# Optimization experiments

Hardware: AMD Instinct MI355X
Metric: run time of the kernel (lower is better)

## Reference

```python
import jax, jax.numpy as jnp
import numpy as np

B, S, D = 4, 2048, 768
H = 12
DH = D // H
NUM_WAY = 4
DFF = 4 * D  # FFN expansion scale=4
EPS = 1e-6


def setup_inputs() -> dict:
    key = jax.random.key(0)
    ks = jax.random.split(key, 20)
    s = 0.02
    inp = {
        "x": jax.random.normal(ks[0], (B, S, D), jnp.float32),
        "w": jax.random.randint(ks[1], (B, S), 0, NUM_WAY, jnp.int64),
        # LayerNorm 1
        "ln1_g": jnp.ones((D,), jnp.float32),
        "ln1_b": jnp.zeros((D,), jnp.float32),
        # Multi-head attention projections (input_dim=out_dim=D)
        "wq": jax.random.normal(ks[2], (D, D), jnp.float32) * s,
        "bq": jnp.zeros((D,), jnp.float32),
        "wk": jax.random.normal(ks[3], (D, D), jnp.float32) * s,
        "bk": jnp.zeros((D,), jnp.float32),
        "wv": jax.random.normal(ks[4], (D, D), jnp.float32) * s,
        "bv": jnp.zeros((D,), jnp.float32),
        "wo": jax.random.normal(ks[5], (D, D), jnp.float32) * s,
        "bo": jnp.zeros((D,), jnp.float32),
        # Way classifier
        "wcls": jax.random.normal(ks[6], (D, NUM_WAY), jnp.float32) * s,
        "bcls": jnp.zeros((NUM_WAY,), jnp.float32),
        # num_way stacked FFN experts: Linear(D,4D) -> ReLU -> Linear(4D,D)
        "w1": jax.random.normal(ks[7], (NUM_WAY, D, DFF), jnp.float32) * s,
        "b1": jnp.zeros((NUM_WAY, DFF), jnp.float32),
        "w2": jax.random.normal(ks[8], (NUM_WAY, DFF, D), jnp.float32) * s,
        "b2": jnp.zeros((NUM_WAY, D), jnp.float32),
    }
    return inp


def _layernorm(x, g, b):
    mu = jnp.mean(x, axis=-1, keepdims=True)
    var = jnp.mean(jnp.square(x - mu), axis=-1, keepdims=True)
    return (x - mu) * jax.lax.rsqrt(var + EPS) * g + b


def reference(x, w, ln1_g, ln1_b, wq, bq, wk, bk, wv, bv, wo, bo,
              wcls, bcls, w1, b1, w2, b2):
    # pre-LN
    xn = _layernorm(x, ln1_g, ln1_b)
    # multi-head self-attention (q = k = v = xn)
    q = (xn @ wq + bq).reshape(B, S, H, DH)
    k = (xn @ wk + bk).reshape(B, S, H, DH)
    v = (xn @ wv + bv).reshape(B, S, H, DH)
    scores = jnp.einsum('bqhd,bkhd->bhqk', q, k) / jnp.sqrt(jnp.float32(DH))
    attn = jax.nn.softmax(scores, axis=-1)
    ctx = jnp.einsum('bhqk,bkhd->bqhd', attn, v).reshape(B, S, D)
    ctx = ctx @ wo + bo
    # dropout is identity at inference; residual
    out = ctx + x
    # dense compute-all-experts FFN, then per-token select by routing id w
    # (mask-overwrite in original == one-hot select since masks partition)
    ffn_out = jnp.zeros_like(out)
    for ci in range(NUM_WAY):
        h = jax.nn.relu(out @ w1[ci] + b1[ci])        # [B,S,4D]
        fi = h @ w2[ci] + b2[ci]                      # [B,S,D]
        mask = (w == ci).astype(out.dtype)[..., None]  # [B,S,1]
        if ci == 0:
            # original initializes ffn_out with way-0 output everywhere;
            # later ways overwrite where w == ci, net = select expert w
            ffn_out = fi
        else:
            ffn_out = ffn_out * (1.0 - mask) + fi * mask
    way_logits = out @ wcls + bcls  # [B,S,NUM_WAY]
    return ffn_out, way_logits
```

## Files before the change

kernel.cpp:

```cpp
#include <hip/hip_runtime.h>
#include <cstdint>

typedef unsigned short u16;
typedef float f32x4 __attribute__((ext_vector_type(4)));
typedef float f32x16 __attribute__((ext_vector_type(16)));
typedef __bf16 bf16x8 __attribute__((ext_vector_type(8)));

#define LOG2E 1.44269504088896340736f

__device__ __forceinline__ u16 f2bf(float f) {
    union { float f; unsigned u; } v; v.f = f;
    unsigned r = v.u + 0x7fffu + ((v.u >> 16) & 1u);
    return (u16)(r >> 16);
}

__device__ __forceinline__ unsigned cvt_pk_bf16(float lo, float hi) {
    unsigned r;
    asm("v_cvt_pk_bf16_f32 %0, %1, %2" : "=v"(r) : "v"(lo), "v"(hi));
    return r;
}

__device__ __forceinline__ float exp2_hw(float x) {
    float r;
    asm("v_exp_f32 %0, %1" : "=v"(r) : "v"(x));
    return r;
}

__device__ __forceinline__ f32x4 mfma16(bf16x8 a, bf16x8 b, f32x4 c) {
    return __builtin_amdgcn_mfma_f32_16x16x32_bf16(a, b, c, 0, 0, 0);
}

__device__ __forceinline__ f32x16 mfma32(bf16x8 a, bf16x8 b, f32x16 c) {
    return __builtin_amdgcn_mfma_f32_32x32x16_bf16(a, b, c, 0, 0, 0);
}

__device__ __forceinline__ void gload_lds16(const void* g, void* l) {
    __builtin_amdgcn_global_load_lds(
        (__attribute__((address_space(1))) unsigned int*)(g),
        (__attribute__((address_space(3))) unsigned int*)(l),
        16, 0, 0);
}

#define MB_TOK 8192
#define DM 768
#define HH 12
#define DHD 64
#define NWAY 4
#define DFF 3072
#define SEQ 2048
#define NBATCH 4

__global__ __launch_bounds__(256) void ln_kernel(
    const float* __restrict__ x, const float* __restrict__ g,
    const float* __restrict__ bb, u16* __restrict__ xn)
{
    int row = blockIdx.x, t = threadIdx.x;
    const float* xr = x + (size_t)row * DM;
    float v0 = xr[t], v1 = xr[t + 256], v2 = xr[t + 512];
    float s = v0 + v1 + v2;
    __shared__ float red[4];
    #pragma unroll
    for (int k = 1; k < 64; k <<= 1) s += __shfl_xor(s, k);
    if ((t & 63) == 0) red[t >> 6] = s;
    __syncthreads();
    float mu = (red[0] + red[1] + red[2] + red[3]) * (1.f / 768.f);
    float d0 = v0 - mu, d1 = v1 - mu, d2 = v2 - mu;
    float q = d0 * d0 + d1 * d1 + d2 * d2;
    #pragma unroll
    for (int k = 1; k < 64; k <<= 1) q += __shfl_xor(q, k);
    __syncthreads();
    if ((t & 63) == 0) red[t >> 6] = q;
    __syncthreads();
    float var = (red[0] + red[1] + red[2] + red[3]) * (1.f / 768.f);
    float rs = rsqrtf(var + 1e-6f);
    u16* xo = xn + (size_t)row * DM;
    xo[t]       = f2bf(d0 * rs * g[t]       + bb[t]);
    xo[t + 256] = f2bf(d1 * rs * g[t + 256] + bb[t + 256]);
    xo[t + 512] = f2bf(d2 * rs * g[t + 512] + bb[t + 512]);
}

__global__ __launch_bounds__(256) void transpose_bf16(
    const float* __restrict__ src, u16* __restrict__ dst, int K, int N)
{
    __shared__ float tl[32][33];
    size_t bofs = (size_t)blockIdx.z * K * N;
    src += bofs; dst += bofs;
    int n0 = blockIdx.x * 32, k0 = blockIdx.y * 32;
    int tx = threadIdx.x, ty = threadIdx.y;
    #pragma unroll
    for (int j = 0; j < 4; ++j)
        tl[ty + j * 8][tx] = src[(size_t)(k0 + ty + j * 8) * N + n0 + tx];
    __syncthreads();
    #pragma unroll
    for (int j = 0; j < 4; ++j)
        dst[(size_t)(n0 + ty + j * 8) * K + k0 + tx] = f2bf(tl[tx][ty + j * 8]);
}

__global__ __launch_bounds__(256) void vT_kernel(
    const u16* __restrict__ qkv, u16* __restrict__ vT)
{
    __shared__ u16 tl[32][33];
    int bh = blockIdx.z;
    int b = bh / HH, h = bh % HH;
    int key0 = blockIdx.x * 32;
    int d0 = blockIdx.y * 32;
    int tx = threadIdx.x, ty = threadIdx.y;
    const u16* src = qkv + ((size_t)b * SEQ + key0) * 2304 + 1536 + h * 64 + d0;
    #pragma unroll
    for (int j = 0; j < 4; ++j)
        tl[ty + j * 8][tx] = src[(size_t)(ty + j * 8) * 2304 + tx];
    __syncthreads();
    u16* dst = vT + ((size_t)bh * 64 + d0) * SEQ + key0;
    #pragma unroll
    for (int j = 0; j < 4; ++j)
        dst[(size_t)(ty + j * 8) * SEQ + tx] = tl[tx][ty + j * 8];
}

__global__ void concat_bias_kernel(const float* bq, const float* bk,
                                   const float* bv, float* bqkv)
{
    int i = blockIdx.x * 256 + threadIdx.x;
    if (i < 2304) bqkv[i] = i < 768 ? bq[i] : (i < 1536 ? bk[i - 768] : bv[i - 1536]);
}

__global__ void route_kernel(const int* __restrict__ wl,
                             int* __restrict__ perm, int* __restrict__ eoff,
                             int4* __restrict__ fmap, int4* __restrict__ fmap64)
{
    __shared__ int cnt[4], cur[4], off[5];
    int tid = threadIdx.x;
    if (tid < 4) cnt[tid] = 0;
    __syncthreads();
    for (int t = tid; t < MB_TOK; t += 256) atomicAdd(&cnt[wl[t] & 3], 1);
    __syncthreads();
    if (tid == 0) {
        off[0] = 0;
        for (int e = 0; e < 4; ++e) off[e + 1] = off[e] + cnt[e];
        int idx = 0;
        for (int e = 0; e < 4; ++e)
            for (int s = 0; s < cnt[e]; s += 128)
                fmap[idx++] = make_int4(e, off[e], s, cnt[e] - s);
        for (; idx < 72; ++idx) fmap[idx] = make_int4(-1, 0, 0, 0);
        int idx2 = 0;
        for (int e = 0; e < 4; ++e)
            for (int s = 0; s < cnt[e]; s += 64)
                fmap64[idx2++] = make_int4(e, off[e], s, cnt[e] - s);
        for (; idx2 < 136; ++idx2) fmap64[idx2] = make_int4(-1, 0, 0, 0);
        for (int e = 0; e < 5; ++e) eoff[e] = off[e];
        for (int e = 0; e < 4; ++e) cur[e] = off[e];
    }
    __syncthreads();
    for (int t = tid; t < MB_TOK; t += 256) {
        int e = wl[t] & 3;
        int pos = atomicAdd(&cur[e], 1);
        perm[pos] = t;
    }
}

template<int MODE, int TM, bool RELU, bool RES, bool ST32, bool ST16>
__global__ __launch_bounds__(256, (TM == 64) ? 4 : 3) void gemm_bt_kernel(
    const u16* __restrict__ A, const u16* __restrict__ Bt,
    const float* __restrict__ bias, const float* __restrict__ res,
    float* __restrict__ out32, u16* __restrict__ out16,
    int nbt, int N, int K, int ntn,
    const int* __restrict__ perm, const int4* __restrict__ fmap)
{
    constexpr int ALD = TM * 32;
    constexpr int BLD = 128 * 32;
    constexpr int NLD = (TM == 128) ? 4 : 3;
    constexpr int NN  = (TM == 64) ? 2 : 4;
    __shared__ __attribute__((aligned(16))) u16 As[3][ALD];
    __shared__ __attribute__((aligned(16))) u16 Bs[3][BLD];
    int tid = threadIdx.x;
    int wv = tid >> 6, ln = tid & 63;
    int bpx = gridDim.x / (ntn << 3);
    int jj = blockIdx.x >> 3;
    int bt = (blockIdx.x & 7) * bpx + jj / ntn;
    int tn = (jj % ntn) * 128;
    if (bt >= nbt) return;

    int seg = 0, ms = 0, mb = TM, tm = 0;
    if (MODE != 0) {
        int4 ent = fmap[bt];
        if (ent.x < 0) return;
        seg = ent.y; ms = ent.z; mb = ent.w; if (mb > TM) mb = TM;
        Bt += (size_t)ent.x * N * K;
        bias += ent.x * N;
    } else {
        tm = bt * TM;
    }

    f32x4 acc[4][NN];
    #pragma unroll
    for (int i = 0; i < 4; ++i)
        #pragma unroll
        for (int j = 0; j < NN; ++j) acc[i][j] = f32x4{0.f, 0.f, 0.f, 0.f};

    int wr = (TM == 128) ? (wv >> 1) : 0;
    int wcol0 = (TM == 128) ? (wv & 1) * 64 : wv * 32;
    int lr = ln & 15, hi = ln >> 4;
    int nk = K / 32;

    const u16* asrc[2];
    const u16* bsrc[2];
    #pragma unroll
    for (int i = 0; i < 2; ++i) {
        int rb2 = (TM == 128) ? ((wv * 2 + i) * 16 + (ln >> 2))
                              : (wv * 16 + (ln >> 2));
        if (TM == 128 || i == 0) {
            int am = rb2 < mb ? rb2 : (mb - 1);
            size_t arow;
            if (MODE == 1)      arow = (size_t)perm[seg + ms + am];
            else if (MODE == 2) arow = (size_t)(seg + ms + am);
            else                arow = (size_t)(tm + rb2);
            asrc[i] = A + arow * K + (ln & 3) * 8;
        }
        int rB = (wv * 2 + i) * 16 + (ln >> 2);
        bsrc[i] = Bt + (size_t)(tn + rB) * K + (ln & 3) * 8;
    }
    int aofs0 = (TM == 128) ? (wv * 2) * 512 : wv * 512;
    int bofs0 = (wv * 2) * 512, bofs1 = (wv * 2 + 1) * 512;

#define GSTAGE(ab_, bb_, k0_) do {                                        \
    gload_lds16(asrc[0] + (k0_), (ab_) + aofs0);                          \
    if (TM == 128) gload_lds16(asrc[1] + (k0_), (ab_) + aofs0 + 512);     \
    gload_lds16(bsrc[0] + (k0_), (bb_) + bofs0);                          \
    gload_lds16(bsrc[1] + (k0_), (bb_) + bofs1);                          \
} while (0)

    u16* A0 = &As[0][0];
    u16* B0 = &Bs[0][0];
    GSTAGE(A0, B0, 0);
    GSTAGE(A0 + ALD, B0 + BLD, 32);
    int bf3 = 0;
    for (int kk = 0; kk < nk; ++kk) {
        if (kk + 1 < nk)
            asm volatile("s_waitcnt vmcnt(%0) lgkmcnt(0)" :: "i"(NLD) : "memory");
        else
            asm volatile("s_waitcnt vmcnt(0) lgkmcnt(0)" ::: "memory");
        __builtin_amdgcn_s_barrier();
        __builtin_amdgcn_sched_barrier(0);
        if (kk + 2 < nk) {
            int nb = bf3 + 2; if (nb >= 3) nb -= 3;
            GSTAGE(A0 + nb * ALD, B0 + nb * BLD, (kk + 2) * 32);
        }
        const u16* Ab = A0 + bf3 * ALD;
        const u16* Bb = B0 + bf3 * BLD;
        bf16x8 a[4], b[NN];
        #pragma unroll
        for (int m = 0; m < 4; ++m)
            a[m] = *(const bf16x8*)&Ab[(wr * 64 + m * 16 + lr) * 32 + hi * 8];
        #pragma unroll
        for (int n = 0; n < NN; ++n)
            b[n] = *(const bf16x8*)&Bb[(wcol0 + n * 16 + lr) * 32 + hi * 8];
        #pragma unroll
        for (int m = 0; m < 4; ++m)
            #pragma unroll
            for (int n = 0; n < NN; ++n)
                acc[m][n] = mfma16(a[m], b[n], acc[m][n]);
        bf3 = (bf3 == 2) ? 0 : bf3 + 1;
    }
#undef GSTAGE

    #pragma unroll
    for (int m = 0; m < 4; ++m) {
        int rb = wr * 64 + m * 16 + hi * 4;
        #pragma unroll
        for (int n = 0; n < NN; ++n) {
            int gcol = tn + wcol0 + n * 16 + lr;
            float bvv = bias[gcol];
            #pragma unroll
            for (int i = 0; i < 4; ++i) {
                int rml = rb + i;
                float v = acc[m][n][i] + bvv;
                if (RELU) v = v > 0.f ? v : 0.f;
                if (MODE == 0) {
                    size_t grow = (size_t)(tm + rml);
                    if (RES) v += res[grow * N + gcol];
                    if (ST32) out32[grow * N + gcol] = v;
                    if (ST16) out16[grow * N + gcol] = f2bf(v);
                } else {
                    if (rml < mb) {
                        size_t orow = (MODE == 1) ? (size_t)(seg + ms + rml)
                                                  : (size_t)perm[seg + ms + rml];
                        if (ST32) out32[orow * N + gcol] = v;
                        if (ST16) out16[orow * N + gcol] = f2bf(v);
                    }
                }
            }
        }
    }
}

__global__ __launch_bounds__(256, 4) void attn_kernel(
    const u16* __restrict__ qkv, const u16* __restrict__ vT,
    u16* __restrict__ ctx)
{
    __shared__ __attribute__((aligned(16))) u16 Ks[2][4096];
    __shared__ __attribute__((aligned(16))) u16 Vs[2][4096];
    int tid = threadIdx.x;
    int wv = tid >> 6, ln = tid & 63;
    int qv = ln & 31, hi = ln >> 5;
    int bid = blockIdx.x;
    int bh = (bid & 7) * 6 + ((bid >> 3) % 6);
    int qt = (bid >> 3) / 6;
    int b = bh / HH, h = bh % HH;
    int q0 = qt * 128 + wv * 32;
    size_t qrowb = (size_t)(b * SEQ + q0);
    const float C = 0.125f * LOG2E;

    bf16x8 qf[4];
    {
        const u16* qp = qkv + (qrowb + qv) * 2304 + h * 64 + hi * 8;
        #pragma unroll
        for (int ds = 0; ds < 4; ++ds) qf[ds] = *(const bf16x8*)(qp + ds * 16);
    }

    int csrc = 8 * ((ln & 7) ^ (ln >> 3));
    const size_t kbase = (size_t)b * SEQ * 2304 + 768 + h * 64;
    const u16* vtb = vT + (size_t)bh * 64 * SEQ;
    const u16* kp0 = qkv + kbase + (size_t)(wv * 16 + (ln >> 3)) * 2304 + csrc;
    const u16* kp1 = kp0 + (size_t)8 * 2304;
    const u16* vp0 = vtb + (size_t)(wv * 16 + (ln >> 3)) * SEQ + csrc;
    const u16* vp1 = vp0 + (size_t)8 * SEQ;

#define ATTN_STAGE(bf_, t_) do {                                          \
    gload_lds16(kp0 + (size_t)(t_) * 64 * 2304, &Ks[bf_][(wv * 2) * 512]);\
    gload_lds16(kp1 + (size_t)(t_) * 64 * 2304, &Ks[bf_][(wv * 2 + 1) * 512]);\
    gload_lds16(vp0 + (size_t)(t_) * 64, &Vs[bf_][(wv * 2) * 512]);       \
    gload_lds16(vp1 + (size_t)(t_) * 64, &Vs[bf_][(wv * 2 + 1) * 512]);   \
} while (0)

    f32x16 oacc[2];
    #pragma unroll
    for (int i = 0; i < 2; ++i)
        #pragma unroll
        for (int r = 0; r < 16; ++r) oacc[i][r] = 0.f;
    float m_run = -INFINITY, l_run = 0.f;
    int ksw = (qv & 7) * 8;

    ATTN_STAGE(0, 0);

    for (int kt = 0; kt < SEQ / 64; ++kt) {
        int bf = kt & 1;
        __syncthreads();
        if (kt + 1 < SEQ / 64) ATTN_STAGE(bf ^ 1, kt + 1);

        f32x16 s0, s1;
        #pragma unroll
        for (int r = 0; r < 16; ++r) { s0[r] = 0.f; s1[r] = 0.f; }
        #pragma unroll
        for (int ds = 0; ds < 4; ++ds) {
            bf16x8 ka0 = *(const bf16x8*)&Ks[bf][qv * 64 + ((ds * 16 + hi * 8) ^ ksw)];
            bf16x8 ka1 = *(const bf16x8*)&Ks[bf][(32 + qv) * 64 + ((ds * 16 + hi * 8) ^ ksw)];
            s0 = mfma32(ka0, qf[ds], s0);
            s1 = mfma32(ka1, qf[ds], s1);
        }

        float tmax = s0[0];
        #pragma unroll
        for (int r = 1; r < 16; ++r) tmax = fmaxf(tmax, s0[r]);
        #pragma unroll
        for (int r = 0; r < 16; ++r) tmax = fmaxf(tmax, s1[r]);
        tmax = fmaxf(tmax, __shfl_xor(tmax, 32));

        if (!__all(tmax - m_run <= 64.f)) {
            float m_new = fmaxf(m_run, tmax);
            float corr = exp2_hw((m_run - m_new) * C);
            l_run *= corr;
            #pragma unroll
            for (int i = 0; i < 2; ++i)
                #pragma unroll
                for (int r = 0; r < 16; ++r) oacc[i][r] *= corr;
            m_run = m_new;
        }
        float c2 = -m_run * C;
        float psum = 0.f;
        #pragma unroll
        for (int r = 0; r < 16; ++r) {
            s0[r] = exp2_hw(fmaf(s0[r], C, c2)); psum += s0[r];
            s1[r] = exp2_hw(fmaf(s1[r], C, c2)); psum += s1[r];
        }
        l_run += psum;

        #pragma unroll
        for (int kb = 0; kb < 2; ++kb) {
            #pragma unroll
            for (int hc = 0; hc < 2; ++hc) {
                const f32x16& sv = kb ? s1 : s0;
                unsigned x0 = cvt_pk_bf16(sv[8 * hc + 0], sv[8 * hc + 1]);
                unsigned x1 = cvt_pk_bf16(sv[8 * hc + 2], sv[8 * hc + 3]);
                unsigned x2 = cvt_pk_bf16(sv[8 * hc + 4], sv[8 * hc + 5]);
                unsigned x3 = cvt_pk_bf16(sv[8 * hc + 6], sv[8 * hc + 7]);
                unsigned t0 = hi ? x0 : x2, t1 = hi ? x1 : x3;
                unsigned r0 = (unsigned)__shfl_xor((int)t0, 32);
                unsigned r1 = (unsigned)__shfl_xor((int)t1, 32);
                union { bf16x8 v; unsigned u[4]; } pf;
                pf.u[0] = hi ? r0 : x0; pf.u[1] = hi ? r1 : x1;
                pf.u[2] = hi ? x2 : r0; pf.u[3] = hi ? x3 : r1;
                int kc = (kb * 32 + hc * 16 + hi * 8) ^ ksw;
                #pragma unroll
                for (int dblk = 0; dblk < 2; ++dblk) {
                    bf16x8 va = *(const bf16x8*)&Vs[bf][(dblk * 32 + qv) * 64 + kc];
                    oacc[dblk] = mfma32(va, pf.v, oacc[dblk]);
                }
            }
        }
    }
#undef ATTN_STAGE

    float l_tot = l_run + __shfl_xor(l_run, 32);
    float inv = 1.f / l_tot;

    __syncthreads();
    u16* eb = &Ks[0][0] + wv * 2048;
    #pragma unroll
    for (int dblk = 0; dblk < 2; ++dblk)
        #pragma unroll
        for (int r = 0; r < 16; r += 2) {
            int d = dblk * 32 + (r & 3) + 8 * (r >> 2) + 4 * hi;
            unsigned pk = cvt_pk_bf16(oacc[dblk][r] * inv, oacc[dblk][r + 1] * inv);
            *(unsigned*)&eb[qv * 64 + (d ^ ((qv & 7) * 8))] = pk;
        }
    __syncthreads();
    {
        u16* ctr = ctx + (qrowb + qv) * DM + h * 64 + hi * 32;
        #pragma unroll
        for (int g = 0; g < 4; ++g) {
            bf16x8 vv = *(const bf16x8*)&eb[qv * 64 + ((hi * 32 + g * 8) ^ ((qv & 7) * 8))];
            *(bf16x8*)(ctr + g * 8) = vv;
        }
    }
}

__global__ __launch_bounds__(256) void cls_kernel(
    const float* __restrict__ outm, const float* __restrict__ wcls,
    const float* __restrict__ bcls, float* __restrict__ dst)
{
    int row = blockIdx.x, t = threadIdx.x;
    const float* xr = outm + (size_t)row * DM;
    float a0 = 0, a1 = 0, a2 = 0, a3 = 0;
    for (int j = t; j < DM; j += 256) {
        float xv = xr[j];
        float4 wv4 = *(const float4*)(const void*)(wcls + (size_t)j * 4);
        a0 += xv * wv4.x; a1 += xv * wv4.y; a2 += xv * wv4.z; a3 += xv * wv4.w;
    }
    #pragma unroll
    for (int k = 1; k < 64; k <<= 1) {
        a0 += __shfl_xor(a0, k); a1 += __shfl_xor(a1, k);
        a2 += __shfl_xor(a2, k); a3 += __shfl_xor(a3, k);
    }
    __shared__ float red[4][4];
    if ((t & 63) == 0) {
        int wid = t >> 6;
        red[wid][0] = a0; red[wid][1] = a1; red[wid][2] = a2; red[wid][3] = a3;
    }
    __syncthreads();
    if (t < 4)
        dst[(size_t)row * 4 + t] =
            red[0][t] + red[1][t] + red[2][t] + red[3][t] + bcls[t];
}

extern "C" void kernel_launch(void* const* d_in, const int* in_sizes, int n_in,
                              void* d_out, int out_size, void* d_ws, size_t ws_size,
                              hipStream_t stream) {
    const float* x      = (const float*)d_in[0];
    const int*   wl     = (const int*)d_in[1];
    const float* ln_g   = (const float*)d_in[2];
    const float* ln_b   = (const float*)d_in[3];
    const float* wq     = (const float*)d_in[4];
    const float* bq     = (const float*)d_in[5];
    const float* wk     = (const float*)d_in[6];
    const float* bk     = (const float*)d_in[7];
    const float* wvv    = (const float*)d_in[8];
    const float* bv     = (const float*)d_in[9];
    const float* wo     = (const float*)d_in[10];
    const float* bo     = (const float*)d_in[11];
    const float* wcls   = (const float*)d_in[12];
    const float* bcls   = (const float*)d_in[13];
    const float* w1     = (const float*)d_in[14];
    const float* b1     = (const float*)d_in[15];
    const float* w2     = (const float*)d_in[16];
    const float* b2     = (const float*)d_in[17];
    float* out = (float*)d_out;

    char* ws = (char*)d_ws;
    u16*   xn    = (u16*)  (ws + 0);
    u16*   qkv   = (u16*)  (ws + 12582912);
    u16*   hbuf  = (u16*)  (ws + 0);
    u16*   ctx   = (u16*)  (ws + 50331648);
    u16*   outb  = (u16*)  (ws + 62914560);
    u16*   wqkvt = (u16*)  (ws + 75497472);
    u16*   wot   = (u16*)  (ws + 79036416);
    u16*   w1t   = (u16*)  (ws + 80216064);
    u16*   w2t   = (u16*)  (ws + 99090432);
    float* bqkv  = (float*)(ws + 117964800);
    int*   perm  = (int*)  (ws + 117974016);
    int*   eoff  = (int*)  (ws + 118006784);
    int4*  fmap  = (int4*) (ws + 118006816);
    int4*  fmap64= (int4*) (ws + 118007968);
    u16*   vT    = (u16*)  (ws + 118010144);
    float* outf  = out;

    route_kernel<<<1, 256, 0, stream>>>(wl, perm, eoff, fmap, fmap64);
    concat_bias_kernel<<<9, 256, 0, stream>>>(bq, bk, bv, bqkv);
    dim3 tb(32, 8);
    transpose_bf16<<<dim3(24, 24, 1), tb, 0, stream>>>(wq,  wqkvt,             768, 768);
    transpose_bf16<<<dim3(24, 24, 1), tb, 0, stream>>>(wk,  wqkvt + 768 * 768, 768, 768);
    transpose_bf16<<<dim3(24, 24, 1), tb, 0, stream>>>(wvv, wqkvt + 2 * 768 * 768, 768, 768);
    transpose_bf16<<<dim3(24, 24, 1), tb, 0, stream>>>(wo,  wot, 768, 768);
    transpose_bf16<<<dim3(96, 24, 4), tb, 0, stream>>>(w1,  w1t, 768, 3072);
    transpose_bf16<<<dim3(24, 96, 4), tb, 0, stream>>>(w2,  w2t, 3072, 768);
    ln_kernel<<<MB_TOK, 256, 0, stream>>>(x, ln_g, ln_b, xn);

    gemm_bt_kernel<0, 128, false, false, false, true><<<1152, 256, 0, stream>>>(
        xn, wqkvt, bqkv, nullptr, nullptr, qkv, 64, 2304, 768, 18, nullptr, nullptr);

    vT_kernel<<<dim3(64, 2, 48), tb, 0, stream>>>(qkv, vT);

    attn_kernel<<<768, 256, 0, stream>>>(qkv, vT, ctx);

    gemm_bt_kernel<0, 64, false, true, true, true><<<768, 256, 0, stream>>>(
        ctx, wot, bo, x, outf, outb, 128, 768, 768, 6, nullptr, nullptr);

    cls_kernel<<<MB_TOK, 256, 0, stream>>>(outf, wcls, bcls, out + (size_t)MB_TOK * DM);

    gemm_bt_kernel<1, 128, true, false, false, true><<<1728, 256, 0, stream>>>(
        outb, w1t, b1, nullptr, nullptr, hbuf, 72, DFF, 768, 24, perm, fmap);

    gemm_bt_kernel<2, 64, false, false, true, false><<<816, 256, 0, stream>>>(
        hbuf, w2t, b2, nullptr, out, nullptr, 136, 768, DFF, 6, perm, fmap64);
}
```

Measured before the change: 395.7 us.

## Fuse prep kernels into one launch, switch GEMM to double buffering, drop fp32 residual store

LayerNorm, the weight transposes, bias concatenation and routing now run as one prep kernel dispatched by block-index ranges, replacing nine launches with one. The GEMM moves from a three-stage LDS pipeline with explicit waitcnt to a simpler two-buffer loop using __syncthreads, and occupancy is set to 4 for all tile sizes. The Wo GEMM no longer writes the fp32 residual output, and the classifier reads the bf16 copy instead, which costs classifier precision. The two-buffer loop exposes more load latency per k-step.

```diff
diff --git a/kernel.cpp b/kernel.cpp
--- a/kernel.cpp
+++ b/kernel.cpp
@@ -12,6 +12,10 @@
     union { float f; unsigned u; } v; v.f = f;
     unsigned r = v.u + 0x7fffu + ((v.u >> 16) & 1u);
     return (u16)(r >> 16);
+}
+
+__device__ __forceinline__ float bf2f(u16 v) {
+    union { unsigned u; float f; } x; x.u = ((unsigned)v) << 16; return x.f;
 }
 
 __device__ __forceinline__ unsigned cvt_pk_bf16(float lo, float hi) {
@@ -50,85 +54,94 @@
 #define SEQ 2048
 #define NBATCH 4
 
-__global__ __launch_bounds__(256) void ln_kernel(
-    const float* __restrict__ x, const float* __restrict__ g,
-    const float* __restrict__ bb, u16* __restrict__ xn)
-{
-    int row = blockIdx.x, t = threadIdx.x;
-    const float* xr = x + (size_t)row * DM;
-    float v0 = xr[t], v1 = xr[t + 256], v2 = xr[t + 512];
-    float s = v0 + v1 + v2;
-    __shared__ float red[4];
-    #pragma unroll
-    for (int k = 1; k < 64; k <<= 1) s += __shfl_xor(s, k);
-    if ((t & 63) == 0) red[t >> 6] = s;
-    __syncthreads();
-    float mu = (red[0] + red[1] + red[2] + red[3]) * (1.f / 768.f);
-    float d0 = v0 - mu, d1 = v1 - mu, d2 = v2 - mu;
-    float q = d0 * d0 + d1 * d1 + d2 * d2;
-    #pragma unroll
-    for (int k = 1; k < 64; k <<= 1) q += __shfl_xor(q, k);
-    __syncthreads();
-    if ((t & 63) == 0) red[t >> 6] = q;
-    __syncthreads();
-    float var = (red[0] + red[1] + red[2] + red[3]) * (1.f / 768.f);
-    float rs = rsqrtf(var + 1e-6f);
-    u16* xo = xn + (size_t)row * DM;
-    xo[t]       = f2bf(d0 * rs * g[t]       + bb[t]);
-    xo[t + 256] = f2bf(d1 * rs * g[t + 256] + bb[t + 256]);
-    xo[t + 512] = f2bf(d2 * rs * g[t + 512] + bb[t + 512]);
-}
-
-__global__ __launch_bounds__(256) void transpose_bf16(
-    const float* __restrict__ src, u16* __restrict__ dst, int K, int N)
+#define PREP_LN_END   8192
+#define PREP_T7_END   10496
+#define PREP_W1_END   19712
+#define PREP_W2_END   28928
+#define PREP_CB_END   28937
+#define PREP_GRID     28938
+
+__global__ __launch_bounds__(256) void prep_kernel(
+    const float* __restrict__ x, const float* __restrict__ ln_g,
+    const float* __restrict__ ln_b, u16* __restrict__ xn,
+    const float* __restrict__ wq, const float* __restrict__ wk,
+    const float* __restrict__ wvv, const float* __restrict__ wo,
+    u16* __restrict__ wqkvt, u16* __restrict__ wot,
+    const float* __restrict__ w1, u16* __restrict__ w1t,
+    const float* __restrict__ w2, u16* __restrict__ w2t,
+    const float* __restrict__ bq, const float* __restrict__ bk,
+    const float* __restrict__ bv, float* __restrict__ bqkv,
+    const int* __restrict__ wl, int* __restrict__ perm,
+    int* __restrict__ eoff, int4* __restrict__ fmap, int4* __restrict__ fmap64)
 {
     __shared__ float tl[32][33];
-    size_t bofs = (size_t)blockIdx.z * K * N;
-    src += bofs; dst += bofs;
-    int n0 = blockIdx.x * 32, k0 = blockIdx.y * 32;
-    int tx = threadIdx.x, ty = threadIdx.y;
-    #pragma unroll
-    for (int j = 0; j < 4; ++j)
-        tl[ty + j * 8][tx] = src[(size_t)(k0 + ty + j * 8) * N + n0 + tx];
-    __syncthreads();
-    #pragma unroll
-    for (int j = 0; j < 4; ++j)
-        dst[(size_t)(n0 + ty + j * 8) * K + k0 + tx] = f2bf(tl[tx][ty + j * 8]);
-}
-
-__global__ __launch_bounds__(256) void vT_kernel(
-    const u16* __restrict__ qkv, u16* __restrict__ vT)
-{
-    __shared__ u16 tl[32][33];
-    int bh = blockIdx.z;
-    int b = bh / HH, h = bh % HH;
-    int key0 = blockIdx.x * 32;
-    int d0 = blockIdx.y * 32;
-    int tx = threadIdx.x, ty = threadIdx.y;
-    const u16* src = qkv + ((size_t)b * SEQ + key0) * 2304 + 1536 + h * 64 + d0;
-    #pragma unroll
-    for (int j = 0; j < 4; ++j)
-        tl[ty + j * 8][tx] = src[(size_t)(ty + j * 8) * 2304 + tx];
-    __syncthreads();
-    u16* dst = vT + ((size_t)bh * 64 + d0) * SEQ + key0;
-    #pragma unroll
-    for (int j = 0; j < 4; ++j)
-        dst[(size_t)(ty + j * 8) * SEQ + tx] = tl[tx][ty + j * 8];
-}
-
-__global__ void concat_bias_kernel(const float* bq, const float* bk,
-                                   const float* bv, float* bqkv)
-{
-    int i = blockIdx.x * 256 + threadIdx.x;
-    if (i < 2304) bqkv[i] = i < 768 ? bq[i] : (i < 1536 ? bk[i - 768] : bv[i - 1536]);
-}
-
-__global__ void route_kernel(const int* __restrict__ wl,
-                             int* __restrict__ perm, int* __restrict__ eoff,
-                             int4* __restrict__ fmap, int4* __restrict__ fmap64)
-{
+    __shared__ float red[4];
     __shared__ int cnt[4], cur[4], off[5];
-    int tid = threadIdx.x;
+    int bid = blockIdx.x, tid = threadIdx.x;
+
+    if (bid < PREP_LN_END) {
+        int row = bid;
+        const float* xr = x + (size_t)row * DM;
+        float v0 = xr[tid], v1 = xr[tid + 256], v2 = xr[tid + 512];
+        float s = v0 + v1 + v2;
+        #pragma unroll
+        for (int k = 1; k < 64; k <<= 1) s += __shfl_xor(s, k);
+        if ((tid & 63) == 0) red[tid >> 6] = s;
+        __syncthreads();
+        float mu = (red[0] + red[1] + red[2] + red[3]) * (1.f / 768.f);
+        float d0 = v0 - mu, d1 = v1 - mu, d2 = v2 - mu;
+        float q = d0 * d0 + d1 * d1 + d2 * d2;
+        #pragma unroll
+        for (int k = 1; k < 64; k <<= 1) q += __shfl_xor(q, k);
+        __syncthreads();
+        if ((tid & 63) == 0) red[tid >> 6] = q;
+        __syncthreads();
+        float var = (red[0] + red[1] + red[2] + red[3]) * (1.f / 768.f);
+        float rs = rsqrtf(var + 1e-6f);
+        u16* xo = xn + (size_t)row * DM;
+        xo[tid]       = f2bf(d0 * rs * ln_g[tid]       + ln_b[tid]);
+        xo[tid + 256] = f2bf(d1 * rs * ln_g[tid + 256] + ln_b[tid + 256]);
+        xo[tid + 512] = f2bf(d2 * rs * ln_g[tid + 512] + ln_b[tid + 512]);
+        return;
+    }
+    if (bid < PREP_W2_END) {
+        const float* src; u16* dst; int K, N, n0, k0;
+        if (bid < PREP_T7_END) {
+            int r = bid - PREP_LN_END;
+            int wsel = r / 576, lb = r % 576;
+            K = 768; N = 768;
+            n0 = (lb % 24) * 32; k0 = (lb / 24) * 32;
+            src = wsel == 0 ? wq : (wsel == 1 ? wk : (wsel == 2 ? wvv : wo));
+            dst = wsel == 3 ? wot : (wqkvt + (size_t)wsel * 768 * 768);
+        } else if (bid < PREP_W1_END) {
+            int lb = bid - PREP_T7_END;
+            K = 768; N = 3072;
+            n0 = (lb % 96) * 32; k0 = ((lb / 96) % 24) * 32;
+            int z = lb / 2304;
+            src = w1 + (size_t)z * K * N; dst = w1t + (size_t)z * K * N;
+        } else {
+            int lb = bid - PREP_W1_END;
+            K = 3072; N = 768;
+            n0 = (lb % 24) * 32; k0 = ((lb / 24) % 96) * 32;
+            int z = lb / 2304;
+            src = w2 + (size_t)z * K * N; dst = w2t + (size_t)z * K * N;
+        }
+        int tx = tid & 31, ty = tid >> 5;
+        #pragma unroll
+        for (int j = 0; j < 4; ++j)
+            tl[ty + j * 8][tx] = src[(size_t)(k0 + ty + j * 8) * N + n0 + tx];
+        __syncthreads();
+        #pragma unroll
+        for (int j = 0; j < 4; ++j)
+            dst[(size_t)(n0 + ty + j * 8) * K + k0 + tx] = f2bf(tl[tx][ty + j * 8]);
+        return;
+    }
+    if (bid < PREP_CB_END) {
+        int i = (bid - PREP_W2_END) * 256 + tid;
+        if (i < 2304)
+            bqkv[i] = i < 768 ? bq[i] : (i < 1536 ? bk[i - 768] : bv[i - 1536]);
+        return;
+    }
     if (tid < 4) cnt[tid] = 0;
     __syncthreads();
     for (int t = tid; t < MB_TOK; t += 256) atomicAdd(&cnt[wl[t] & 3], 1);
@@ -157,8 +170,28 @@
     }
 }
 
+__global__ __launch_bounds__(256) void vT_kernel(
+    const u16* __restrict__ qkv, u16* __restrict__ vT)
+{
+    __shared__ u16 tl[32][33];
+    int bh = blockIdx.z;
+    int b = bh / HH, h = bh % HH;
+    int key0 = blockIdx.x * 32;
+    int d0 = blockIdx.y * 32;
+    int tx = threadIdx.x & 31, ty = threadIdx.x >> 5;
+    const u16* src = qkv + ((size_t)b * SEQ + key0) * 2304 + 1536 + h * 64 + d0;
+    #pragma unroll
+    for (int j = 0; j < 4; ++j)
+        tl[ty + j * 8][tx] = src[(size_t)(ty + j * 8) * 2304 + tx];
+    __syncthreads();
+    u16* dst = vT + ((size_t)bh * 64 + d0) * SEQ + key0;
+    #pragma unroll
+    for (int j = 0; j < 4; ++j)
+        dst[(size_t)(ty + j * 8) * SEQ + tx] = tl[tx][ty + j * 8];
+}
+
 template<int MODE, int TM, bool RELU, bool RES, bool ST32, bool ST16>
-__global__ __launch_bounds__(256, (TM == 64) ? 4 : 3) void gemm_bt_kernel(
+__global__ __launch_bounds__(256, 4) void gemm_bt_kernel(
     const u16* __restrict__ A, const u16* __restrict__ Bt,
     const float* __restrict__ bias, const float* __restrict__ res,
     float* __restrict__ out32, u16* __restrict__ out16,
@@ -166,11 +199,9 @@
     const int* __restrict__ perm, const int4* __restrict__ fmap)
 {
     constexpr int ALD = TM * 32;
-    constexpr int BLD = 128 * 32;
-    constexpr int NLD = (TM == 128) ? 4 : 3;
     constexpr int NN  = (TM == 64) ? 2 : 4;
-    __shared__ __attribute__((aligned(16))) u16 As[3][ALD];
-    __shared__ __attribute__((aligned(16))) u16 Bs[3][BLD];
+    __shared__ __attribute__((aligned(16))) u16 As[2][ALD];
+    __shared__ __attribute__((aligned(16))) u16 Bs[2][4096];
     int tid = threadIdx.x;
     int wv = tid >> 6, ln = tid & 63;
     int bpx = gridDim.x / (ntn << 3);
@@ -205,60 +236,45 @@
     const u16* bsrc[2];
     #pragma unroll
     for (int i = 0; i < 2; ++i) {
-        int rb2 = (TM == 128) ? ((wv * 2 + i) * 16 + (ln >> 2))
-                              : (wv * 16 + (ln >> 2));
+        int rA = (TM == 128) ? ((wv * 2 + i) * 16 + (ln >> 2))
+                             : (wv * 16 + (ln >> 2));
         if (TM == 128 || i == 0) {
-            int am = rb2 < mb ? rb2 : (mb - 1);
+            int am = rA < mb ? rA : (mb - 1);
             size_t arow;
             if (MODE == 1)      arow = (size_t)perm[seg + ms + am];
             else if (MODE == 2) arow = (size_t)(seg + ms + am);
-            else                arow = (size_t)(tm + rb2);
+            else                arow = (size_t)(tm + rA);
             asrc[i] = A + arow * K + (ln & 3) * 8;
         }
         int rB = (wv * 2 + i) * 16 + (ln >> 2);
         bsrc[i] = Bt + (size_t)(tn + rB) * K + (ln & 3) * 8;
     }
     int aofs0 = (TM == 128) ? (wv * 2) * 512 : wv * 512;
-    int bofs0 = (wv * 2) * 512, bofs1 = (wv * 2 + 1) * 512;
-
-#define GSTAGE(ab_, bb_, k0_) do {                                        \
-    gload_lds16(asrc[0] + (k0_), (ab_) + aofs0);                          \
-    if (TM == 128) gload_lds16(asrc[1] + (k0_), (ab_) + aofs0 + 512);     \
-    gload_lds16(bsrc[0] + (k0_), (bb_) + bofs0);                          \
-    gload_lds16(bsrc[1] + (k0_), (bb_) + bofs1);                          \
+
+#define GSTAGE(bf_, k0_) do {                                             \
+    gload_lds16(asrc[0] + (k0_), &As[bf_][aofs0]);                        \
+    if (TM == 128) gload_lds16(asrc[1] + (k0_), &As[bf_][aofs0 + 512]);   \
+    gload_lds16(bsrc[0] + (k0_), &Bs[bf_][(wv * 2) * 512]);               \
+    gload_lds16(bsrc[1] + (k0_), &Bs[bf_][(wv * 2 + 1) * 512]);           \
 } while (0)
 
-    u16* A0 = &As[0][0];
-    u16* B0 = &Bs[0][0];
-    GSTAGE(A0, B0, 0);
-    GSTAGE(A0 + ALD, B0 + BLD, 32);
-    int bf3 = 0;
+    GSTAGE(0, 0);
     for (int kk = 0; kk < nk; ++kk) {
-        if (kk + 1 < nk)
-            asm volatile("s_waitcnt vmcnt(%0) lgkmcnt(0)" :: "i"(NLD) : "memory");
-        else
-            asm volatile("s_waitcnt vmcnt(0) lgkmcnt(0)" ::: "memory");
-        __builtin_amdgcn_s_barrier();
-        __builtin_amdgcn_sched_barrier(0);
-        if (kk + 2 < nk) {
-            int nb = bf3 + 2; if (nb >= 3) nb -= 3;
-            GSTAGE(A0 + nb * ALD, B0 + nb * BLD, (kk + 2) * 32);
-        }
-        const u16* Ab = A0 + bf3 * ALD;
-        const u16* Bb = B0 + bf3 * BLD;
+        int bf = kk & 1;
+        __syncthreads();
+        if (kk + 1 < nk) GSTAGE(bf ^ 1, (kk + 1) * 32);
         bf16x8 a[4], b[NN];
         #pragma unroll
         for (int m = 0; m < 4; ++m)
-            a[m] = *(const bf16x8*)&Ab[(wr * 64 + m * 16 + lr) * 32 + hi * 8];
+            a[m] = *(const bf16x8*)&As[bf][(wr * 64 + m * 16 + lr) * 32 + hi * 8];
         #pragma unroll
         for (int n = 0; n < NN; ++n)
-            b[n] = *(const bf16x8*)&Bb[(wcol0 + n * 16 + lr) * 32 + hi * 8];
+            b[n] = *(const bf16x8*)&Bs[bf][(wcol0 + n * 16 + lr) * 32 + hi * 8];
         #pragma unroll
         for (int m = 0; m < 4; ++m)
             #pragma unroll
             for (int n = 0; n < NN; ++n)
                 acc[m][n] = mfma16(a[m], b[n], acc[m][n]);
-        bf3 = (bf3 == 2) ? 0 : bf3 + 1;
     }
 #undef GSTAGE
 
@@ -434,14 +450,14 @@
 }
 
 __global__ __launch_bounds__(256) void cls_kernel(
-    const float* __restrict__ outm, const float* __restrict__ wcls,
+    const u16* __restrict__ outm, const float* __restrict__ wcls,
     const float* __restrict__ bcls, float* __restrict__ dst)
 {
     int row = blockIdx.x, t = threadIdx.x;
-    const float* xr = outm + (size_t)row * DM;
+    const u16* xr = outm + (size_t)row * DM;
     float a0 = 0, a1 = 0, a2 = 0, a3 = 0;
     for (int j = t; j < DM; j += 256) {
-        float xv = xr[j];
+        float xv = bf2f(xr[j]);
         float4 wv4 = *(const float4*)(const void*)(wcls + (size_t)j * 4);
         a0 += xv * wv4.x; a1 += xv * wv4.y; a2 += xv * wv4.z; a3 += xv * wv4.w;
     }
@@ -500,30 +516,22 @@
     int4*  fmap  = (int4*) (ws + 118006816);
     int4*  fmap64= (int4*) (ws + 118007968);
     u16*   vT    = (u16*)  (ws + 118010144);
-    float* outf  = out;
-
-    route_kernel<<<1, 256, 0, stream>>>(wl, perm, eoff, fmap, fmap64);
-    concat_bias_kernel<<<9, 256, 0, stream>>>(bq, bk, bv, bqkv);
-    dim3 tb(32, 8);
-    transpose_bf16<<<dim3(24, 24, 1), tb, 0, stream>>>(wq,  wqkvt,             768, 768);
-    transpose_bf16<<<dim3(24, 24, 1), tb, 0, stream>>>(wk,  wqkvt + 768 * 768, 768, 768);
-    transpose_bf16<<<dim3(24, 24, 1), tb, 0, stream>>>(wvv, wqkvt + 2 * 768 * 768, 768, 768);
-    transpose_bf16<<<dim3(24, 24, 1), tb, 0, stream>>>(wo,  wot, 768, 768);
-    transpose_bf16<<<dim3(96, 24, 4), tb, 0, stream>>>(w1,  w1t, 768, 3072);
-    transpose_bf16<<<dim3(24, 96, 4), tb, 0, stream>>>(w2,  w2t, 3072, 768);
-    ln_kernel<<<MB_TOK, 256, 0, stream>>>(x, ln_g, ln_b, xn);
+
+    prep_kernel<<<PREP_GRID, 256, 0, stream>>>(
+        x, ln_g, ln_b, xn, wq, wk, wvv, wo, wqkvt, wot,
+        w1, w1t, w2, w2t, bq, bk, bv, bqkv, wl, perm, eoff, fmap, fmap64);
 
     gemm_bt_kernel<0, 128, false, false, false, true><<<1152, 256, 0, stream>>>(
         xn, wqkvt, bqkv, nullptr, nullptr, qkv, 64, 2304, 768, 18, nullptr, nullptr);
 
-    vT_kernel<<<dim3(64, 2, 48), tb, 0, stream>>>(qkv, vT);
+    vT_kernel<<<dim3(64, 2, 48), 256, 0, stream>>>(qkv, vT);
 
     attn_kernel<<<768, 256, 0, stream>>>(qkv, vT, ctx);
 
-    gemm_bt_kernel<0, 64, false, true, true, true><<<768, 256, 0, stream>>>(
-        ctx, wot, bo, x, outf, outb, 128, 768, 768, 6, nullptr, nullptr);
-
-    cls_kernel<<<MB_TOK, 256, 0, stream>>>(outf, wcls, bcls, out + (size_t)MB_TOK * DM);
+    gemm_bt_kernel<0, 64, false, true, false, true><<<768, 256, 0, stream>>>(
+        ctx, wot, bo, x, nullptr, outb, 128, 768, 768, 6, nullptr, nullptr);
+
+    cls_kernel<<<MB_TOK, 256, 0, stream>>>(outb, wcls, bcls, out + (size_t)MB_TOK * DM);
 
     gemm_bt_kernel<1, 128, true, false, false, true><<<1728, 256, 0, stream>>>(
         outb, w1t, b1, nullptr, nullptr, hbuf, 72, DFF, 768, 24, perm, fmap);
```

Result: faster. 357.7 us (-9.6%).
